# Kernel optimization log

Measured on AMD Instinct MI355X. Metric: run time of the kernel, lower is better.

## Reference

```python
import jax, jax.numpy as jnp
from jax import lax
import numpy as np


def setup_inputs() -> dict:
    key = jax.random.key(0)
    k1, k2 = jax.random.split(key)
    sat_features = jax.random.normal(k1, (128, 4, 64, 16), dtype=jnp.float32)  # [B_s, h, w, c]
    grd_features = jax.random.normal(k2, (128, 4, 64, 16), dtype=jnp.float32)  # [B_g, h, gw, c]
    return {"sat_features": sat_features, "grd_features": grd_features}


def reference(sat_features, grd_features):
    B_s, h, w, c = sat_features.shape
    B_g, gh, gw, gc = grd_features.shape
    assert h == gh and c == gc

    # --- corr: circular cross-correlation over width via conv2d ---
    n = gw - 1
    sat_pad = jnp.concatenate([sat_features, sat_features[:, :, :n, :]], axis=2)  # [B_s,h,w+n,c]
    rhs = jnp.transpose(grd_features, (1, 2, 3, 0))  # HWIO: [h,gw,c,B_g]
    out = lax.conv_general_dilated(
        sat_pad, rhs, window_strides=(1, 1), padding='VALID',
        dimension_numbers=('NHWC', 'HWIO', 'NHWC'))  # [B_s,1,w,B_g]
    corr = out[:, 0, :, :]                  # [B_s, w, B_g]
    orien = jnp.argmax(corr, axis=1)        # [B_s, B_g] int

    # --- crop_sat: circular-shift gather along width, crop to grd width ---
    shift = orien % w                                                   # [B_s,B_g]
    idx = (jnp.arange(gw)[None, None, :] + shift[:, :, None]) % w       # [B_s,B_g,gw]
    # gather: sat_crop[i,j,y,k,ch] = sat_features[i, y, idx[i,j,k], ch]
    sat_crop = jnp.take_along_axis(
        sat_features[:, None],              # [B_s,1,h,w,c]
        idx[:, :, None, :, None],           # [B_s,B_g,1,gw,1]
        axis=3)                             # -> [B_s,B_g,h,gw,c]

    # --- L2 normalize per (sat,grd) pair and squared-chord distance ---
    norm = jnp.sqrt(jnp.sum(sat_crop * sat_crop, axis=(2, 3, 4), keepdims=True))
    sat_matrix = sat_crop / jnp.maximum(norm, 1e-12)
    dot = jnp.sum(sat_matrix * grd_features[None], axis=(2, 3, 4))      # [B_s,B_g]
    distance = 2.0 - 2.0 * dot.T                                        # [B_g,B_s]

    return sat_features, grd_features, distance, orien
```

## Files before the change

### kernel.cpp

```cpp
#include <hip/hip_runtime.h>
#include <math.h>

typedef _Float16 f16;
typedef __attribute__((ext_vector_type(8))) _Float16 f16x8;
typedef __attribute__((ext_vector_type(16))) float f32x16;

#define DIST_OFF  1048576
#define ORI_OFF   1064960
#define SATP_STR  72

#define MFMA(a,b,c) __builtin_amdgcn_mfma_f32_32x32x16_f16((a),(b),(c),0,0,0)

__global__ __launch_bounds__(256) void prep_k(const float* __restrict__ grd,
                                              f16* __restrict__ gHi, f16* __restrict__ gLo,
                                              const float4* __restrict__ satIn,
                                              const float4* __restrict__ grdIn,
                                              float4* __restrict__ out4) {
    const int b = blockIdx.x;
    if (b >= 64) {
        int i = (b - 64) * 256 + threadIdx.x;
        out4[i] = satIn[i];
        out4[131072 + i] = grdIn[i];
        return;
    }
    __shared__ f16 tH[8192], tL[8192];
    const int tid = threadIdx.x;
    const int g0 = (b & 7) * 16;
    const int kq = b >> 3;
    #pragma unroll
    for (int i = 0; i < 32; ++i) {
        int flat = i * 256 + tid;
        int g_l = flat >> 9;
        int r   = flat & 511;
        int h   = r >> 7;
        int j   = r & 127;
        float v = grd[(((g0 + g_l) * 4 + h) * 64 + kq * 8) * 16 + j];
        int k_l = (j >> 4) * 64 + h * 16 + (j & 15);
        f16 hv = (f16)v;
        int a = (k_l >> 3) * 128 + g_l * 8 + (k_l & 7);
        tH[a] = hv;
        tL[a] = (f16)(v - (float)hv);
    }
    __syncthreads();
    #pragma unroll
    for (int i = 0; i < 4; ++i) {
        int f = i * 256 + tid;
        int dst = (kq * 64 + (f >> 4)) * 128 + g0 + (f & 15);
        ((f16x8*)gHi)[dst] = *(const f16x8*)(tH + f * 8);
        ((f16x8*)gLo)[dst] = *(const f16x8*)(tL + f * 8);
    }
}

__global__ __launch_bounds__(512, 2) void corr_k(const float* __restrict__ sat,
                                                 const f16* __restrict__ gHi,
                                                 const f16* __restrict__ gLo,
                                                 float* __restrict__ out) {
    __shared__ __align__(16) unsigned char smem[131072];
    __shared__ float wred[8];
    __shared__ float rnormS;
    f16* sH = (f16*)smem;
    f16* sL = sH + 127 * SATP_STR;
    float* red = (float*)smem;

    const int tid = threadIdx.x;
    const int s  = blockIdx.x >> 1;
    const int gh = blockIdx.x & 1;
    const int wave = tid >> 6, lane = tid & 63;
    const int m = lane & 31, half = lane >> 5;

    const float* satS = sat + s * 4096;
    float ssq = 0.f;
    #pragma unroll
    for (int r = 0; r < 8; ++r) {
        int idx = r * 512 + tid;
        float v = satS[idx];
        int h = idx >> 10, w = (idx >> 4) & 63, c = idx & 15;
        int col = h * 16 + c;
        f16 hv = (f16)v, lv = (f16)(v - (float)hv);
        sH[w * SATP_STR + col] = hv;
        sL[w * SATP_STR + col] = lv;
        if (w < 63) { sH[(w + 64) * SATP_STR + col] = hv; sL[(w + 64) * SATP_STR + col] = lv; }
        ssq += v * v;
    }
    #pragma unroll
    for (int off = 32; off > 0; off >>= 1) ssq += __shfl_down(ssq, off, 64);
    if (lane == 0) wred[wave] = ssq;
    __syncthreads();
    if (tid == 0) {
        float t = 0.f;
        #pragma unroll
        for (int i = 0; i < 8; ++i) t += wred[i];
        rnormS = 1.f / fmaxf(sqrtf(t), 1e-12f);
    }

    const f16* A0h = sH + m * SATP_STR + half * 8;
    const f16* A0l = sL + m * SATP_STR + half * 8;
    const f16x8* BHp = (const f16x8*)gHi;
    const f16x8* BLp = (const f16x8*)gLo;
    const int ggBase = half * 128 + gh * 64 + m;

    f32x16 z;
    #pragma unroll
    for (int r = 0; r < 16; ++r) z[r] = 0.f;
    f32x16 h00 = z, h01 = z, h10 = z, h11 = z, x00 = z, x01 = z, x10 = z, x11 = z;

    f16x8 ah[2][2], al[2][2], bh[2][2], bl[2][2];

#define LOADT(p, t) { \
    int tc = (t) > 255 ? 255 : (t); \
    int ao = (tc >> 2) * SATP_STR + (tc & 3) * 16; \
    ah[p][0] = *(const f16x8*)(A0h + ao); \
    ah[p][1] = *(const f16x8*)(A0h + ao + 32 * SATP_STR); \
    al[p][0] = *(const f16x8*)(A0l + ao); \
    al[p][1] = *(const f16x8*)(A0l + ao + 32 * SATP_STR); \
    int bu = tc * 256 + ggBase; \
    bh[p][0] = BHp[bu]; bh[p][1] = BHp[bu + 32]; \
    bl[p][0] = BLp[bu]; bl[p][1] = BLp[bu + 32]; }

#define STEP(p) { \
    h00 = MFMA(ah[p][0], bh[p][0], h00); \
    h01 = MFMA(ah[p][0], bh[p][1], h01); \
    h10 = MFMA(ah[p][1], bh[p][0], h10); \
    h11 = MFMA(ah[p][1], bh[p][1], h11); \
    x00 = MFMA(ah[p][0], bl[p][0], x00); x00 = MFMA(al[p][0], bh[p][0], x00); \
    x01 = MFMA(ah[p][0], bl[p][1], x01); x01 = MFMA(al[p][0], bh[p][1], x01); \
    x10 = MFMA(ah[p][1], bl[p][0], x10); x10 = MFMA(al[p][1], bh[p][0], x10); \
    x11 = MFMA(ah[p][1], bl[p][1], x11); x11 = MFMA(al[p][1], bh[p][1], x11); }

    const int t0 = wave * 32;
    LOADT(0, t0)
    #pragma unroll 4
    for (int t = t0; t < t0 + 32; t += 2) {
        LOADT(1, t + 1)
        STEP(0)
        LOADT(0, t + 2)
        STEP(1)
    }
    h00 = h00 + x00; h01 = h01 + x01; h10 = h10 + x10; h11 = h11 + x11;

    __syncthreads();
    float* rw = red + wave * 4096;
    #pragma unroll
    for (int r = 0; r < 16; ++r) {
        int j0 = (r & 3) + 8 * (r >> 2) + 4 * half;
        rw[j0 * 64 + m]             = h00[r];
        rw[j0 * 64 + 32 + m]        = h01[r];
        rw[(j0 + 32) * 64 + m]      = h10[r];
        rw[(j0 + 32) * 64 + 32 + m] = h11[r];
    }
    __syncthreads();
    #pragma unroll
    for (int i = 0; i < 8; ++i) {
        int c = i * 512 + tid;
        float v = red[c]         + red[c + 4096]  + red[c + 8192]  + red[c + 12288]
                + red[c + 16384] + red[c + 20480] + red[c + 24576] + red[c + 28672];
        red[c] = v;
    }
    __syncthreads();

    if (tid < 64) {
        int g = tid;
        float best = red[g];
        int bj = 0;
        for (int j = 1; j < 64; ++j) {
            float v = red[j * 64 + g];
            if (v > best) { best = v; bj = j; }
        }
        float dot = best * rnormS;
        int gg = gh * 64 + g;
        out[DIST_OFF + gg * 128 + s] = 2.f - 2.f * dot;
        out[ORI_OFF + s * 128 + gg]  = (float)bj;
    }
}

__global__ void copy_k(const float4* __restrict__ a, const float4* __restrict__ b,
                       float4* __restrict__ out) {
    int i = blockIdx.x * 256 + threadIdx.x;
    out[i] = a[i];
    out[131072 + i] = b[i];
}

extern "C" void kernel_launch(void* const* d_in, const int* in_sizes, int n_in,
                              void* d_out, int out_size, void* d_ws, size_t ws_size,
                              hipStream_t stream) {
    const float* sat = (const float*)d_in[0];
    const float* grd = (const float*)d_in[1];
    float* out = (float*)d_out;

    const bool useWs = (ws_size >= (size_t)2 * 1024 * 1024);
    f16* gHi;
    f16* gLo;
    if (useWs) {
        gHi = (f16*)d_ws;
        gLo = gHi + 524288;
    } else {
        gHi = (f16*)out;
        gLo = (f16*)(out + 262144);
    }

    prep_k<<<useWs ? 576 : 64, 256, 0, stream>>>(grd, gHi, gLo,
                                                 (const float4*)sat, (const float4*)grd,
                                                 (float4*)out);
    corr_k<<<256, 512, 0, stream>>>(sat, gHi, gLo, out);
    if (!useWs)
        copy_k<<<512, 256, 0, stream>>>((const float4*)sat, (const float4*)grd, (float4*)out);
}
```

Before: 85.37 us.

## Move passthrough copy into corr kernel, deepen B prefetch, vectorize sat staging

The input passthrough copy moves from the prep kernel into the tail of the correlation kernel, so the prep launch shrinks to 64 blocks and the copy overlaps with other blocks' compute. The MFMA loop now loads B tiles three steps ahead with a fully unrolled schedule and raises wave priority around MFMA groups. Sat staging into LDS uses float4 loads and f16x4 stores instead of scalar ones. The trade-off is higher register pressure from the deeper prefetch and full unroll at 2 blocks/CU, plus extra tail work in each corr block.

Result: no change. 86.36 us (+1.2%).

```diff
diff --git a/kernel.cpp b/kernel.cpp
--- a/kernel.cpp
+++ b/kernel.cpp
@@ -2,6 +2,7 @@
 #include <math.h>
 
 typedef _Float16 f16;
+typedef __attribute__((ext_vector_type(4))) _Float16 f16x4;
 typedef __attribute__((ext_vector_type(8))) _Float16 f16x8;
 typedef __attribute__((ext_vector_type(16))) float f32x16;
 
@@ -12,17 +13,8 @@
 #define MFMA(a,b,c) __builtin_amdgcn_mfma_f32_32x32x16_f16((a),(b),(c),0,0,0)
 
 __global__ __launch_bounds__(256) void prep_k(const float* __restrict__ grd,
-                                              f16* __restrict__ gHi, f16* __restrict__ gLo,
-                                              const float4* __restrict__ satIn,
-                                              const float4* __restrict__ grdIn,
-                                              float4* __restrict__ out4) {
+                                              f16* __restrict__ gHi, f16* __restrict__ gLo) {
     const int b = blockIdx.x;
-    if (b >= 64) {
-        int i = (b - 64) * 256 + threadIdx.x;
-        out4[i] = satIn[i];
-        out4[131072 + i] = grdIn[i];
-        return;
-    }
     __shared__ f16 tH[8192], tL[8192];
     const int tid = threadIdx.x;
     const int g0 = (b & 7) * 16;
@@ -54,7 +46,11 @@
 __global__ __launch_bounds__(512, 2) void corr_k(const float* __restrict__ sat,
                                                  const f16* __restrict__ gHi,
                                                  const f16* __restrict__ gLo,
-                                                 float* __restrict__ out) {
+                                                 float* __restrict__ out,
+                                                 const float4* __restrict__ satIn,
+                                                 const float4* __restrict__ grdIn,
+                                                 float4* __restrict__ out4,
+                                                 int doCopy) {
     __shared__ __align__(16) unsigned char smem[131072];
     __shared__ float wred[8];
     __shared__ float rnormS;
@@ -68,19 +64,24 @@
     const int wave = tid >> 6, lane = tid & 63;
     const int m = lane & 31, half = lane >> 5;
 
-    const float* satS = sat + s * 4096;
+    const float4* satS4 = (const float4*)(sat + s * 4096);
     float ssq = 0.f;
     #pragma unroll
-    for (int r = 0; r < 8; ++r) {
-        int idx = r * 512 + tid;
-        float v = satS[idx];
-        int h = idx >> 10, w = (idx >> 4) & 63, c = idx & 15;
-        int col = h * 16 + c;
-        f16 hv = (f16)v, lv = (f16)(v - (float)hv);
-        sH[w * SATP_STR + col] = hv;
-        sL[w * SATP_STR + col] = lv;
-        if (w < 63) { sH[(w + 64) * SATP_STR + col] = hv; sL[(w + 64) * SATP_STR + col] = lv; }
-        ssq += v * v;
+    for (int r = 0; r < 2; ++r) {
+        int i4 = r * 512 + tid;
+        float4 v = satS4[i4];
+        int h = i4 >> 8, w = (i4 >> 2) & 63;
+        int col = h * 16 + (i4 & 3) * 4;
+        f16x4 hq = {(f16)v.x, (f16)v.y, (f16)v.z, (f16)v.w};
+        f16x4 lq = {(f16)(v.x - (float)hq[0]), (f16)(v.y - (float)hq[1]),
+                    (f16)(v.z - (float)hq[2]), (f16)(v.w - (float)hq[3])};
+        *(f16x4*)(sH + w * SATP_STR + col) = hq;
+        *(f16x4*)(sL + w * SATP_STR + col) = lq;
+        if (w < 63) {
+            *(f16x4*)(sH + (w + 64) * SATP_STR + col) = hq;
+            *(f16x4*)(sL + (w + 64) * SATP_STR + col) = lq;
+        }
+        ssq += v.x * v.x + v.y * v.y + v.z * v.z + v.w * v.w;
     }
     #pragma unroll
     for (int off = 32; off > 0; off >>= 1) ssq += __shfl_down(ssq, off, 64);
@@ -104,37 +105,40 @@
     for (int r = 0; r < 16; ++r) z[r] = 0.f;
     f32x16 h00 = z, h01 = z, h10 = z, h11 = z, x00 = z, x01 = z, x10 = z, x11 = z;
 
-    f16x8 ah[2][2], al[2][2], bh[2][2], bl[2][2];
-
-#define LOADT(p, t) { \
-    int tc = (t) > 255 ? 255 : (t); \
-    int ao = (tc >> 2) * SATP_STR + (tc & 3) * 16; \
+    f16x8 ah[2][2], al[2][2], bh[3][2], bl[3][2];
+
+#define LOADA(p, t) { \
+    int ao = ((t) >> 2) * SATP_STR + ((t) & 3) * 16; \
     ah[p][0] = *(const f16x8*)(A0h + ao); \
     ah[p][1] = *(const f16x8*)(A0h + ao + 32 * SATP_STR); \
     al[p][0] = *(const f16x8*)(A0l + ao); \
-    al[p][1] = *(const f16x8*)(A0l + ao + 32 * SATP_STR); \
-    int bu = tc * 256 + ggBase; \
+    al[p][1] = *(const f16x8*)(A0l + ao + 32 * SATP_STR); }
+
+#define LOADB(p, t) { \
+    int bu = (t) * 256 + ggBase; \
     bh[p][0] = BHp[bu]; bh[p][1] = BHp[bu + 32]; \
     bl[p][0] = BLp[bu]; bl[p][1] = BLp[bu + 32]; }
 
-#define STEP(p) { \
-    h00 = MFMA(ah[p][0], bh[p][0], h00); \
-    h01 = MFMA(ah[p][0], bh[p][1], h01); \
-    h10 = MFMA(ah[p][1], bh[p][0], h10); \
-    h11 = MFMA(ah[p][1], bh[p][1], h11); \
-    x00 = MFMA(ah[p][0], bl[p][0], x00); x00 = MFMA(al[p][0], bh[p][0], x00); \
-    x01 = MFMA(ah[p][0], bl[p][1], x01); x01 = MFMA(al[p][0], bh[p][1], x01); \
-    x10 = MFMA(ah[p][1], bl[p][0], x10); x10 = MFMA(al[p][1], bh[p][0], x10); \
-    x11 = MFMA(ah[p][1], bl[p][1], x11); x11 = MFMA(al[p][1], bh[p][1], x11); }
+#define STEP(p, q) { \
+    __builtin_amdgcn_s_setprio(1); \
+    h00 = MFMA(ah[p][0], bh[q][0], h00); \
+    h01 = MFMA(ah[p][0], bh[q][1], h01); \
+    h10 = MFMA(ah[p][1], bh[q][0], h10); \
+    h11 = MFMA(ah[p][1], bh[q][1], h11); \
+    x00 = MFMA(ah[p][0], bl[q][0], x00); x00 = MFMA(al[p][0], bh[q][0], x00); \
+    x01 = MFMA(ah[p][0], bl[q][1], x01); x01 = MFMA(al[p][0], bh[q][1], x01); \
+    x10 = MFMA(ah[p][1], bl[q][0], x10); x10 = MFMA(al[p][1], bh[q][0], x10); \
+    x11 = MFMA(ah[p][1], bl[q][1], x11); x11 = MFMA(al[p][1], bh[q][1], x11); \
+    __builtin_amdgcn_s_setprio(0); }
 
     const int t0 = wave * 32;
-    LOADT(0, t0)
-    #pragma unroll 4
-    for (int t = t0; t < t0 + 32; t += 2) {
-        LOADT(1, t + 1)
-        STEP(0)
-        LOADT(0, t + 2)
-        STEP(1)
+    LOADB(0, t0) LOADB(1, t0 + 1) LOADB(2, t0 + 2)
+    LOADA(0, t0)
+    #pragma unroll
+    for (int tt = 0; tt < 32; ++tt) {
+        if (tt < 31) LOADA((tt + 1) & 1, t0 + tt + 1)
+        STEP(tt & 1, tt % 3)
+        if (tt < 29) LOADB(tt % 3, t0 + tt + 3)
     }
     h00 = h00 + x00; h01 = h01 + x01; h10 = h10 + x10; h11 = h11 + x11;
 
@@ -171,6 +175,12 @@
         out[DIST_OFF + gg * 128 + s] = 2.f - 2.f * dot;
         out[ORI_OFF + s * 128 + gg]  = (float)bj;
     }
+
+    if (doCopy) {
+        int i = blockIdx.x * 512 + tid;
+        out4[i] = satIn[i];
+        out4[131072 + i] = grdIn[i];
+    }
 }
 
 __global__ void copy_k(const float4* __restrict__ a, const float4* __restrict__ b,
@@ -198,10 +208,10 @@
         gLo = (f16*)(out + 262144);
     }
 
-    prep_k<<<useWs ? 576 : 64, 256, 0, stream>>>(grd, gHi, gLo,
-                                                 (const float4*)sat, (const float4*)grd,
-                                                 (float4*)out);
-    corr_k<<<256, 512, 0, stream>>>(sat, gHi, gLo, out);
+    prep_k<<<64, 256, 0, stream>>>(grd, gHi, gLo);
+    corr_k<<<256, 512, 0, stream>>>(sat, gHi, gLo, out,
+                                    (const float4*)sat, (const float4*)grd, (float4*)out,
+                                    useWs ? 1 : 0);
     if (!useWs)
         copy_k<<<512, 256, 0, stream>>>((const float4*)sat, (const float4*)grd, (float4*)out);
 }
```

## Split corr blocks into quarter ground tiles and fold passthrough copy into corr kernel

Applied to the files above, without the earlier changes.

Each corr block now handles 32 ground images instead of 64, doubling the grid to 512 blocks and halving the shared reduction buffer so more blocks fit per CU (launch bounds raised to 4). The MFMA loop is simplified to two accumulator tiles, loading the sat A fragments every step and double-buffering only the B loads. The input passthrough copy moves from extra prep blocks into the tail of corr_k, so prep_k runs only 64 blocks. This aims for better occupancy and overlap, at the cost of redundant sat staging per block and more register pressure under the tighter launch bound.

Measured after the change: 86.88 us. About the same (+1.8%).

```diff
diff --git a/kernel.cpp b/kernel.cpp
--- a/kernel.cpp
+++ b/kernel.cpp
@@ -12,17 +12,8 @@
 #define MFMA(a,b,c) __builtin_amdgcn_mfma_f32_32x32x16_f16((a),(b),(c),0,0,0)
 
 __global__ __launch_bounds__(256) void prep_k(const float* __restrict__ grd,
-                                              f16* __restrict__ gHi, f16* __restrict__ gLo,
-                                              const float4* __restrict__ satIn,
-                                              const float4* __restrict__ grdIn,
-                                              float4* __restrict__ out4) {
+                                              f16* __restrict__ gHi, f16* __restrict__ gLo) {
     const int b = blockIdx.x;
-    if (b >= 64) {
-        int i = (b - 64) * 256 + threadIdx.x;
-        out4[i] = satIn[i];
-        out4[131072 + i] = grdIn[i];
-        return;
-    }
     __shared__ f16 tH[8192], tL[8192];
     const int tid = threadIdx.x;
     const int g0 = (b & 7) * 16;
@@ -51,11 +42,15 @@
     }
 }
 
-__global__ __launch_bounds__(512, 2) void corr_k(const float* __restrict__ sat,
+__global__ __launch_bounds__(512, 4) void corr_k(const float* __restrict__ sat,
                                                  const f16* __restrict__ gHi,
                                                  const f16* __restrict__ gLo,
-                                                 float* __restrict__ out) {
-    __shared__ __align__(16) unsigned char smem[131072];
+                                                 float* __restrict__ out,
+                                                 const float4* __restrict__ satIn,
+                                                 const float4* __restrict__ grdIn,
+                                                 float4* __restrict__ out4,
+                                                 int doCopy) {
+    __shared__ __align__(16) unsigned char smem[65536];
     __shared__ float wred[8];
     __shared__ float rnormS;
     f16* sH = (f16*)smem;
@@ -63,8 +58,8 @@
     float* red = (float*)smem;
 
     const int tid = threadIdx.x;
-    const int s  = blockIdx.x >> 1;
-    const int gh = blockIdx.x & 1;
+    const int s  = blockIdx.x >> 2;
+    const int gq = blockIdx.x & 3;
     const int wave = tid >> 6, lane = tid & 63;
     const int m = lane & 31, half = lane >> 5;
 
@@ -97,79 +92,69 @@
     const f16* A0l = sL + m * SATP_STR + half * 8;
     const f16x8* BHp = (const f16x8*)gHi;
     const f16x8* BLp = (const f16x8*)gLo;
-    const int ggBase = half * 128 + gh * 64 + m;
+    const int bBase = half * 128 + gq * 32 + m;
 
     f32x16 z;
     #pragma unroll
     for (int r = 0; r < 16; ++r) z[r] = 0.f;
-    f32x16 h00 = z, h01 = z, h10 = z, h11 = z, x00 = z, x01 = z, x10 = z, x11 = z;
+    f32x16 h0 = z, h1 = z, x0 = z, x1 = z;
 
-    f16x8 ah[2][2], al[2][2], bh[2][2], bl[2][2];
+    f16x8 a0h, a0l, a1h, a1l, bh[2], bl[2];
 
-#define LOADT(p, t) { \
-    int tc = (t) > 255 ? 255 : (t); \
-    int ao = (tc >> 2) * SATP_STR + (tc & 3) * 16; \
-    ah[p][0] = *(const f16x8*)(A0h + ao); \
-    ah[p][1] = *(const f16x8*)(A0h + ao + 32 * SATP_STR); \
-    al[p][0] = *(const f16x8*)(A0l + ao); \
-    al[p][1] = *(const f16x8*)(A0l + ao + 32 * SATP_STR); \
-    int bu = tc * 256 + ggBase; \
-    bh[p][0] = BHp[bu]; bh[p][1] = BHp[bu + 32]; \
-    bl[p][0] = BLp[bu]; bl[p][1] = BLp[bu + 32]; }
-
-#define STEP(p) { \
-    h00 = MFMA(ah[p][0], bh[p][0], h00); \
-    h01 = MFMA(ah[p][0], bh[p][1], h01); \
-    h10 = MFMA(ah[p][1], bh[p][0], h10); \
-    h11 = MFMA(ah[p][1], bh[p][1], h11); \
-    x00 = MFMA(ah[p][0], bl[p][0], x00); x00 = MFMA(al[p][0], bh[p][0], x00); \
-    x01 = MFMA(ah[p][0], bl[p][1], x01); x01 = MFMA(al[p][0], bh[p][1], x01); \
-    x10 = MFMA(ah[p][1], bl[p][0], x10); x10 = MFMA(al[p][1], bh[p][0], x10); \
-    x11 = MFMA(ah[p][1], bl[p][1], x11); x11 = MFMA(al[p][1], bh[p][1], x11); }
+#define LOADB(p, t) { int bu = (t) * 256 + bBase; bh[p] = BHp[bu]; bl[p] = BLp[bu]; }
+#define LOADA(t) { int ao = ((t) >> 2) * SATP_STR + ((t) & 3) * 16; \
+    a0h = *(const f16x8*)(A0h + ao); a0l = *(const f16x8*)(A0l + ao); \
+    a1h = *(const f16x8*)(A0h + ao + 32 * SATP_STR); \
+    a1l = *(const f16x8*)(A0l + ao + 32 * SATP_STR); }
 
     const int t0 = wave * 32;
-    LOADT(0, t0)
-    #pragma unroll 4
-    for (int t = t0; t < t0 + 32; t += 2) {
-        LOADT(1, t + 1)
-        STEP(0)
-        LOADT(0, t + 2)
-        STEP(1)
+    LOADB(0, t0)
+    #pragma unroll
+    for (int tt = 0; tt < 32; ++tt) {
+        if (tt < 31) LOADB((tt + 1) & 1, t0 + tt + 1)
+        LOADA(t0 + tt)
+        h0 = MFMA(a0h, bh[tt & 1], h0);
+        h1 = MFMA(a1h, bh[tt & 1], h1);
+        x0 = MFMA(a0h, bl[tt & 1], x0); x0 = MFMA(a0l, bh[tt & 1], x0);
+        x1 = MFMA(a1h, bl[tt & 1], x1); x1 = MFMA(a1l, bh[tt & 1], x1);
     }
-    h00 = h00 + x00; h01 = h01 + x01; h10 = h10 + x10; h11 = h11 + x11;
+    f32x16 p0 = h0 + x0, p1 = h1 + x1;
 
     __syncthreads();
-    float* rw = red + wave * 4096;
+    float* rw = red + wave * 2048;
     #pragma unroll
     for (int r = 0; r < 16; ++r) {
         int j0 = (r & 3) + 8 * (r >> 2) + 4 * half;
-        rw[j0 * 64 + m]             = h00[r];
-        rw[j0 * 64 + 32 + m]        = h01[r];
-        rw[(j0 + 32) * 64 + m]      = h10[r];
-        rw[(j0 + 32) * 64 + 32 + m] = h11[r];
+        rw[j0 * 32 + m]        = p0[r];
+        rw[(j0 + 32) * 32 + m] = p1[r];
     }
     __syncthreads();
     #pragma unroll
-    for (int i = 0; i < 8; ++i) {
+    for (int i = 0; i < 4; ++i) {
         int c = i * 512 + tid;
-        float v = red[c]         + red[c + 4096]  + red[c + 8192]  + red[c + 12288]
-                + red[c + 16384] + red[c + 20480] + red[c + 24576] + red[c + 28672];
+        float v = red[c]          + red[c + 2048]  + red[c + 4096]  + red[c + 6144]
+                + red[c + 8192]   + red[c + 10240] + red[c + 12288] + red[c + 14336];
         red[c] = v;
     }
     __syncthreads();
 
-    if (tid < 64) {
+    if (tid < 32) {
         int g = tid;
         float best = red[g];
         int bj = 0;
         for (int j = 1; j < 64; ++j) {
-            float v = red[j * 64 + g];
+            float v = red[j * 32 + g];
             if (v > best) { best = v; bj = j; }
         }
         float dot = best * rnormS;
-        int gg = gh * 64 + g;
+        int gg = gq * 32 + g;
         out[DIST_OFF + gg * 128 + s] = 2.f - 2.f * dot;
         out[ORI_OFF + s * 128 + gg]  = (float)bj;
+    }
+
+    if (doCopy) {
+        int i = blockIdx.x * 512 + tid;
+        out4[i] = (i < 131072) ? satIn[i] : grdIn[i - 131072];
     }
 }
 
@@ -198,10 +183,10 @@
         gLo = (f16*)(out + 262144);
     }
 
-    prep_k<<<useWs ? 576 : 64, 256, 0, stream>>>(grd, gHi, gLo,
-                                                 (const float4*)sat, (const float4*)grd,
-                                                 (float4*)out);
-    corr_k<<<256, 512, 0, stream>>>(sat, gHi, gLo, out);
+    prep_k<<<64, 256, 0, stream>>>(grd, gHi, gLo);
+    corr_k<<<512, 512, 0, stream>>>(sat, gHi, gLo, out,
+                                    (const float4*)sat, (const float4*)grd, (float4*)out,
+                                    useWs ? 1 : 0);
     if (!useWs)
         copy_k<<<512, 256, 0, stream>>>((const float4*)sat, (const float4*)grd, (float4*)out);
 }
```
